# Kernel tuning notes

Hardware: AMD Instinct MI355X
Metric: run time of the kernel (lower is better)

Reference implementation:

```python
import jax, jax.numpy as jnp
import numpy as np

D_MODEL = 1024
N_HEADS = 16
HEAD = D_MODEL // N_HEADS  # 64


def setup_inputs() -> dict:
    key = jax.random.key(0)
    ks = jax.random.split(key, 9)
    s = 1.0 / np.sqrt(D_MODEL)
    x = jax.random.normal(ks[0], (2, 2048, D_MODEL), dtype=jnp.float32)
    Wq = jax.random.uniform(ks[1], (N_HEADS, D_MODEL, HEAD), jnp.float32, -s, s)
    bq = jax.random.uniform(ks[2], (N_HEADS, HEAD), jnp.float32, -s, s)
    Wk = jax.random.uniform(ks[3], (N_HEADS, D_MODEL, HEAD), jnp.float32, -s, s)
    bk = jax.random.uniform(ks[4], (N_HEADS, HEAD), jnp.float32, -s, s)
    Wv = jax.random.uniform(ks[5], (N_HEADS, D_MODEL, HEAD), jnp.float32, -s, s)
    bv = jax.random.uniform(ks[6], (N_HEADS, HEAD), jnp.float32, -s, s)
    Wo = jax.random.uniform(ks[7], (D_MODEL, D_MODEL), jnp.float32, -s, s)
    bo = jax.random.uniform(ks[8], (D_MODEL,), jnp.float32, -s, s)
    return {"x": x, "Wq": Wq, "bq": bq, "Wk": Wk, "bk": bk,
            "Wv": Wv, "bv": bv, "Wo": Wo, "bo": bo}


def reference(x, Wq, bq, Wk, bk, Wv, bv, Wo, bo):
    # Per-head projections, vectorized over heads: [B,S,D] x [H,D,h] -> [B,H,S,h]
    Q = jnp.einsum('bsd,hdk->bhsk', x, Wq) + bq[None, :, None, :]
    K = jnp.einsum('bsd,hdk->bhsk', x, Wk) + bk[None, :, None, :]
    V = jnp.einsum('bsd,hdk->bhsk', x, Wv) + bv[None, :, None, :]
    scores = jnp.einsum('bhqk,bhsk->bhqs', Q, K) / jnp.sqrt(jnp.float32(HEAD))
    attn = jax.nn.softmax(scores, axis=-1)  # dropout is identity in eval mode
    out = jnp.einsum('bhqs,bhsk->bhqk', attn, V)  # [B,H,S,h]
    B, H, S, h = out.shape
    out = out.transpose(0, 2, 1, 3).reshape(B, S, H * h)  # concat heads -> [B,S,D]
    return out @ Wo.T + bo if False else jnp.einsum('bsd,ed->bse', out, Wo.T.T) + bo
```

## Files before the change

### kernel.cpp

```cpp
#include <hip/hip_runtime.h>
#include <hip/hip_bf16.h>

typedef unsigned short u16;
typedef short short8 __attribute__((ext_vector_type(8)));
typedef float floatx4 __attribute__((ext_vector_type(4)));

#define MFMA16(a, b, c) __builtin_amdgcn_mfma_f32_16x16x32_bf16((a), (b), (c), 0, 0, 0)

union U128u { uint4 q; u16 s[8]; };

__device__ __forceinline__ u16 f2bf(float f) {
  union { float f; unsigned u; } v; v.f = f;
  unsigned r = v.u + 0x7fffu + ((v.u >> 16) & 1u);
  return (u16)(r >> 16);
}

__device__ __forceinline__ float bf2f(u16 s) {
  union { unsigned u; float f; } v; v.u = ((unsigned)s) << 16;
  return v.f;
}

__device__ __forceinline__ unsigned pk2(float hi, float lo) {
  union { float f; unsigned u; } a, b;
  a.f = hi; b.f = lo;
  return __builtin_amdgcn_perm(a.u + 0x8000u, b.u + 0x8000u, 0x07060302u);
}

__device__ __forceinline__ float fexp2(float x) {
#if __has_builtin(__builtin_amdgcn_exp2f)
  return __builtin_amdgcn_exp2f(x);
#else
  return exp2f(x);
#endif
}

__device__ __forceinline__ void async16(const u16* g, u16* l) {
  __builtin_amdgcn_global_load_lds(
      (const __attribute__((address_space(1))) unsigned int*)g,
      (__attribute__((address_space(3))) unsigned int*)l, 16, 0, 0);
}


__global__ __launch_bounds__(256) void prep_all(
    const float* __restrict__ x, const float* __restrict__ Wo,
    const float* __restrict__ Wq, const float* __restrict__ bq,
    const float* __restrict__ Wk, const float* __restrict__ bk,
    const float* __restrict__ Wv, const float* __restrict__ bv,
    u16* __restrict__ Xb, u16* __restrict__ Wob,
    u16* __restrict__ Wt, float* __restrict__ ball) {
  int bid = blockIdx.x;
  int tid = threadIdx.x;
  if (bid < 5120) {
    const float* src = bid < 4096 ? x : Wo;
    u16* dst = bid < 4096 ? Xb : Wob;
    int i = (bid < 4096 ? bid : bid - 4096) * 256 + tid;
    float4 v = ((const float4*)src)[i];
    union { unsigned long long ll; u16 s[4]; } o;
    o.s[0] = f2bf(v.x); o.s[1] = f2bf(v.y); o.s[2] = f2bf(v.z); o.s[3] = f2bf(v.w);
    ((unsigned long long*)dst)[i] = o.ll;
    return;
  }
  int id = (bid - 5120) * 256 + tid;
  int kk4 = id & 15;
  int d = (id >> 4) & 1023;
  int h = (id >> 14) & 15;
  int wsel = id >> 18;
  const float* W = wsel == 0 ? Wq : (wsel == 1 ? Wk : Wv);
  float4 v = *(const float4*)(W + ((size_t)(h * 1024 + d)) * 64 + kk4 * 4);
  int nb = wsel * 1024 + h * 64 + kk4 * 4;
  Wt[(size_t)(nb + 0) * 1024 + d] = f2bf(v.x);
  Wt[(size_t)(nb + 1) * 1024 + d] = f2bf(v.y);
  Wt[(size_t)(nb + 2) * 1024 + d] = f2bf(v.z);
  Wt[(size_t)(nb + 3) * 1024 + d] = f2bf(v.w);
  if (id < 3072) {
    int ws2 = id >> 10, hk = id & 1023;
    const float* bsrc = ws2 == 0 ? bq : (ws2 == 1 ? bk : bv);
    ball[id] = bsrc[hk];
  }
}


__device__ __forceinline__ void store_out(u16* p, float v) { *p = f2bf(v); }
__device__ __forceinline__ void store_out(float* p, float v) { *p = v; }

template <int BN, bool SPLITV, bool TRANS, typename OutT>
__global__ __launch_bounds__(256, 4) void gemm_bt(
    const u16* __restrict__ A, const u16* __restrict__ B,
    const float* __restrict__ bias, OutT* __restrict__ C,
    u16* __restrict__ Vtc,
    int M, int N, int K, int scaleNend, float scaleVal) {
  constexpr int TN = BN / 32;
  __shared__ __attribute__((aligned(16))) u16 As[128 * 64];
  __shared__ __attribute__((aligned(16))) u16 Bs[BN * 64];
  const int tid = threadIdx.x;
  const int w = tid >> 6, lane = tid & 63;
  const int l15 = lane & 15, l4 = lane >> 4;
  const int lin = blockIdx.x;
  const int xcd = lin & 7, sblk = lin >> 3;
  const int bm = xcd * 4 + (sblk & 3);
  const int bn = sblk >> 2;
  const int wm = (w & 1) * 64, wn = (w >> 1) * (BN / 2);

  floatx4 acc[4][TN];
#pragma unroll
  for (int i = 0; i < 4; ++i)
#pragma unroll
    for (int j = 0; j < TN; ++j) acc[i][j] = (floatx4){0.f, 0.f, 0.f, 0.f};

  for (int k0 = 0; k0 < K; k0 += 64) {
    __syncthreads();
#pragma unroll
    for (int j = 0; j < 4; ++j) {
      int i = j * 256 + tid;
      int row = i >> 3, c = (i & 7) ^ (row & 7);
      async16(A + (size_t)(bm * 128 + row) * K + k0 + c * 8, As + (j * 256 + w * 64) * 8);
    }
#pragma unroll
    for (int j = 0; j < BN / 32; ++j) {
      int i = j * 256 + tid;
      int row = i >> 3, c = (i & 7) ^ (row & 7);
      async16(B + (size_t)(bn * BN + row) * K + k0 + c * 8, Bs + (j * 256 + w * 64) * 8);
    }
    __syncthreads();
    const int sw = l15 & 7;
#pragma unroll
    for (int ks = 0; ks < 2; ++ks) {
      short8 af[4], bf[TN];
#pragma unroll
      for (int t = 0; t < 4; ++t)
        af[t] = *(const short8*)(As + (wm + t * 16 + l15) * 64 + (((ks * 4 + l4) ^ sw)) * 8);
#pragma unroll
      for (int t = 0; t < TN; ++t)
        bf[t] = *(const short8*)(Bs + (wn + t * 16 + l15) * 64 + (((ks * 4 + l4) ^ sw)) * 8);
#pragma unroll
      for (int tm = 0; tm < 4; ++tm)
#pragma unroll
        for (int tn = 0; tn < TN; ++tn)
          acc[tm][tn] = TRANS ? MFMA16(bf[tn], af[tm], acc[tm][tn])
                              : MFMA16(af[tm], bf[tn], acc[tm][tn]);
    }
  }

  if (TRANS) {
#pragma unroll
    for (int tn = 0; tn < TN; ++tn) {
      int colb = bn * BN + wn + tn * 16 + l4 * 4;
      float4 bv4 = *(const float4*)(bias + colb);
#pragma unroll
      for (int tm = 0; tm < 4; ++tm) {
        int row = bm * 128 + wm + tm * 16 + l15;
        float4 v;
        v.x = acc[tm][tn][0] + bv4.x;
        v.y = acc[tm][tn][1] + bv4.y;
        v.z = acc[tm][tn][2] + bv4.z;
        v.w = acc[tm][tn][3] + bv4.w;
        *(float4*)((float*)C + (size_t)row * N + colb) = v;
      }
    }
    return;
  }

#pragma unroll
  for (int tn = 0; tn < TN; ++tn) {
    int col = bn * BN + wn + tn * 16 + l15;
    float bv = bias[col];
    float sc = (col < scaleNend) ? scaleVal : 1.0f;
    if (!SPLITV || col < 2048) {
#pragma unroll
      for (int tm = 0; tm < 4; ++tm) {
        int row0 = bm * 128 + wm + tm * 16 + l4 * 4;
#pragma unroll
        for (int r = 0; r < 4; ++r) {
          float v = (acc[tm][tn][r] + bv) * sc;
          store_out(C + (size_t)(row0 + r) * N + col, v);
        }
      }
    } else {
      int hv = (col - 2048) >> 6, d = (col - 2048) & 63;
#pragma unroll
      for (int tm = 0; tm < 4; ++tm) {
        int row0 = bm * 128 + wm + tm * 16 + l4 * 4;
        int bb = row0 >> 11, s0 = row0 & 2047;
        union { unsigned long long ll; u16 s[4]; } o;
#pragma unroll
        for (int r = 0; r < 4; ++r) o.s[r] = f2bf(acc[tm][tn][r] + bv);
        size_t idx = ((((size_t)(bb * 16 + hv) * 128 + (s0 >> 4)) * 2 + ((s0 >> 3) & 1)) * 64 + d) * 8 +
                     (s0 & 7);
        *(unsigned long long*)(Vtc + idx) = o.ll;
      }
    }
  }
}

__global__ __launch_bounds__(256, 4) void gemm_out64(
    const u16* __restrict__ A, const u16* __restrict__ B,
    const float* __restrict__ bias, float* __restrict__ C) {
  __shared__ __attribute__((aligned(16))) u16 As[64 * 64];
  __shared__ __attribute__((aligned(16))) u16 Bs[64 * 64];
  const int tid = threadIdx.x;
  const int w = tid >> 6, lane = tid & 63;
  const int l15 = lane & 15, l4 = lane >> 4;
  const int lin = blockIdx.x;
  const int xcd = lin & 7, sblk = lin >> 3;
  const int bm = xcd * 8 + (sblk & 7);
  const int bn = sblk >> 3;
  const int wm = (w & 1) * 32, wn = (w >> 1) * 32;

  floatx4 acc[2][2];
#pragma unroll
  for (int i = 0; i < 2; ++i)
#pragma unroll
    for (int j = 0; j < 2; ++j) acc[i][j] = (floatx4){0.f, 0.f, 0.f, 0.f};

  for (int k0 = 0; k0 < 1024; k0 += 64) {
    __syncthreads();
#pragma unroll
    for (int j = 0; j < 2; ++j) {
      int i = j * 256 + tid;
      int row = i >> 3, c = (i & 7) ^ (row & 7);
      async16(A + (size_t)(bm * 64 + row) * 1024 + k0 + c * 8, As + (j * 256 + w * 64) * 8);
    }
#pragma unroll
    for (int j = 0; j < 2; ++j) {
      int i = j * 256 + tid;
      int row = i >> 3, c = (i & 7) ^ (row & 7);
      async16(B + (size_t)(bn * 64 + row) * 1024 + k0 + c * 8, Bs + (j * 256 + w * 64) * 8);
    }
    __syncthreads();
    const int sw = l15 & 7;
#pragma unroll
    for (int ks = 0; ks < 2; ++ks) {
      short8 af[2], bf[2];
#pragma unroll
      for (int t = 0; t < 2; ++t)
        af[t] = *(const short8*)(As + (wm + t * 16 + l15) * 64 + (((ks * 4 + l4) ^ sw)) * 8);
#pragma unroll
      for (int t = 0; t < 2; ++t)
        bf[t] = *(const short8*)(Bs + (wn + t * 16 + l15) * 64 + (((ks * 4 + l4) ^ sw)) * 8);
#pragma unroll
      for (int tm = 0; tm < 2; ++tm)
#pragma unroll
        for (int tn = 0; tn < 2; ++tn)
          acc[tm][tn] = MFMA16(bf[tn], af[tm], acc[tm][tn]);
    }
  }

#pragma unroll
  for (int tn = 0; tn < 2; ++tn) {
    int colb = bn * 64 + wn + tn * 16 + l4 * 4;
    float4 bv4 = *(const float4*)(bias + colb);
#pragma unroll
    for (int tm = 0; tm < 2; ++tm) {
      int row = bm * 64 + wm + tm * 16 + l15;
      float4 v;
      v.x = acc[tm][tn][0] + bv4.x;
      v.y = acc[tm][tn][1] + bv4.y;
      v.z = acc[tm][tn][2] + bv4.z;
      v.w = acc[tm][tn][3] + bv4.w;
      *(float4*)(C + (size_t)row * 1024 + colb) = v;
    }
  }
}

__global__ __launch_bounds__(256, 3) void attn_kernel(const u16* __restrict__ QKV,
                                                      const u16* __restrict__ Vtc,
                                                      u16* __restrict__ Ob) {
  __shared__ __attribute__((aligned(16))) u16 lds[4 * 5120];
  const int tid = threadIdx.x;
  const int w = tid >> 6, lane = tid & 63;
  const int l15 = lane & 15, l4 = lane >> 4;
  const int lin = blockIdx.x;
  const int xcd = lin & 7, sblk = lin >> 3;
  const int bh = xcd * 4 + (sblk & 3);
  const int q0 = (sblk >> 2) * 64;
  const int b = bh >> 4, h = bh & 15;

  u16* const Pw = lds + w * 5120;

  short8 qf[4][2];
  {
    const u16* Qb = QKV + (size_t)(b * 2048 + q0) * 3072 + h * 64;
#pragma unroll
    for (int tq = 0; tq < 4; ++tq)
#pragma unroll
      for (int s = 0; s < 2; ++s)
        qf[tq][s] = *(const short8*)(Qb + (size_t)(tq * 16 + l15) * 3072 + s * 32 + l4 * 8);
  }

  floatx4 Oacc[4][4];
#pragma unroll
  for (int i = 0; i < 4; ++i)
#pragma unroll
    for (int j = 0; j < 4; ++j) Oacc[i][j] = (floatx4){0.f, 0.f, 0.f, 0.f};
  float lpart[4] = {0.f, 0.f, 0.f, 0.f};

  const u16* const Kb = QKV + (size_t)(b * 2048) * 3072 + 1024 + h * 64;
  const u16* const Vw = Vtc + (size_t)bh * 131072 + (size_t)w * 32768;
  const int kw0 = w * 512;

  auto load_kf = [&](int c, short8 kf[2][2]) {
    const int key0 = kw0 + c * 32;
#pragma unroll
    for (int t = 0; t < 2; ++t)
#pragma unroll
      for (int s = 0; s < 2; ++s)
        kf[t][s] = *(const short8*)(Kb + (size_t)(key0 + t * 16 + l15) * 3072 + s * 32 + l4 * 8);
  };

  auto do_st = [&](const short8 kf[2][2], u16* pb) {
#pragma unroll
    for (int t = 0; t < 2; ++t)
#pragma unroll
      for (int tq = 0; tq < 4; ++tq) {
        floatx4 s = (floatx4){0.f, 0.f, 0.f, 0.f};
        s = MFMA16(kf[t][0], qf[tq][0], s);
        s = MFMA16(kf[t][1], qf[tq][1], s);
        float p0 = fexp2(s[0]), p1 = fexp2(s[1]), p2 = fexp2(s[2]), p3 = fexp2(s[3]);
        lpart[tq] += (p0 + p1) + (p2 + p3);
        unsigned lo = pk2(p1, p0), hi = pk2(p3, p2);
        *(unsigned long long*)(pb + (size_t)(tq * 16 + l15) * 40 + t * 16 + l4 * 4) =
            ((unsigned long long)hi << 32) | lo;
      }
  };

  auto do_pv = [&](int c, const u16* pb) {
    short8 vf[4];
#pragma unroll
    for (int td = 0; td < 4; ++td)
      vf[td] = *(const short8*)(Vw + (size_t)c * 2048 + l4 * 512 + (td * 16 + l15) * 8);
    short8 pf[4];
#pragma unroll
    for (int tq = 0; tq < 4; ++tq)
      pf[tq] = *(const short8*)(pb + (size_t)(tq * 16 + l15) * 40 + l4 * 8);
#pragma unroll
    for (int td = 0; td < 4; ++td)
#pragma unroll
      for (int tq = 0; tq < 4; ++tq) Oacc[tq][td] = MFMA16(pf[tq], vf[td], Oacc[tq][td]);
  };

  short8 kfc[2][2];
  load_kf(0, kfc);
  {
    short8 kfn[2][2];
    load_kf(1, kfn);
    do_st(kfc, Pw);
#pragma unroll
    for (int t = 0; t < 2; ++t)
#pragma unroll
      for (int s = 0; s < 2; ++s) kfc[t][s] = kfn[t][s];
  }
#pragma unroll 1
  for (int c = 1; c < 15; ++c) {
    short8 kfn[2][2];
    load_kf(c + 1, kfn);
    do_st(kfc, Pw + (c & 1) * 2560);
    do_pv(c - 1, Pw + ((c - 1) & 1) * 2560);
#pragma unroll
    for (int t = 0; t < 2; ++t)
#pragma unroll
      for (int s = 0; s < 2; ++s) kfc[t][s] = kfn[t][s];
  }
  do_st(kfc, Pw + 2560);
  do_pv(14, Pw);
  do_pv(15, Pw + 2560);

  float lr[4];
#pragma unroll
  for (int tq = 0; tq < 4; ++tq) {
    float l = lpart[tq];
    l += __shfl_xor(l, 16);
    l += __shfl_xor(l, 32);
    lr[tq] = l;
  }

#pragma unroll
  for (int tq = 0; tq < 4; ++tq)
#pragma unroll
    for (int td = 0; td < 4; ++td)
#pragma unroll
      for (int r = 0; r < 4; ++r)
        Pw[(size_t)(tq * 16 + l4 * 4 + r) * 72 + td * 16 + l15] = f2bf(Oacc[tq][td][r]);
  if (l4 == 0) {
    float* Lw = (float*)(Pw + 4608);
#pragma unroll
    for (int tq = 0; tq < 4; ++tq) Lw[tq * 16 + l15] = lr[tq];
  }
  __syncthreads();

  {
    int row = tid >> 2, c0 = (tid & 3) * 16;
    float acc[16];
#pragma unroll
    for (int j = 0; j < 16; ++j) acc[j] = 0.f;
    float lsum = 0.f;
#pragma unroll
    for (int wv = 0; wv < 4; ++wv) {
      const u16* R = lds + wv * 5120;
      lsum += ((const float*)(R + 4608))[row];
      U128u x1, x2;
      x1.q = *(const uint4*)(R + (size_t)row * 72 + c0);
      x2.q = *(const uint4*)(R + (size_t)row * 72 + c0 + 8);
#pragma unroll
      for (int j = 0; j < 8; ++j) { acc[j] += bf2f(x1.s[j]); acc[8 + j] += bf2f(x2.s[j]); }
    }
    float inv = 1.0f / lsum;
    U128u o1, o2;
#pragma unroll
    for (int j = 0; j < 8; ++j) { o1.s[j] = f2bf(acc[j] * inv); o2.s[j] = f2bf(acc[8 + j] * inv); }
    u16* Op = Ob + (size_t)(b * 2048 + q0 + row) * 1024 + h * 64 + c0;
    *(uint4*)Op = o1.q;
    *(uint4*)(Op + 8) = o2.q;
  }
}


extern "C" void kernel_launch(void* const* d_in, const int* in_sizes, int n_in,
                              void* d_out, int out_size, void* d_ws, size_t ws_size,
                              hipStream_t stream) {
  const float* x  = (const float*)d_in[0];
  const float* Wq = (const float*)d_in[1];
  const float* bq = (const float*)d_in[2];
  const float* Wk = (const float*)d_in[3];
  const float* bk = (const float*)d_in[4];
  const float* Wv = (const float*)d_in[5];
  const float* bv = (const float*)d_in[6];
  const float* Wo = (const float*)d_in[7];
  const float* bo = (const float*)d_in[8];

  char* p = (char*)d_ws;
  u16* Xb   = (u16*)p; p += (size_t)4096 * 1024 * 2;
  u16* Wt   = (u16*)p; p += (size_t)3072 * 1024 * 2;
  u16* QKV  = (u16*)p; p += (size_t)4096 * 3072 * 2;
  u16* Vtc  = (u16*)p; p += (size_t)32 * 128 * 2 * 64 * 8 * 2;
  u16* Ob   = (u16*)p; p += (size_t)4096 * 1024 * 2;
  u16* Wob  = (u16*)p; p += (size_t)1024 * 1024 * 2;
  float* ball = (float*)p; p += 3072 * sizeof(float);

  const float qscale = 0.125f * 1.4426950408889634f;

  prep_all<<<8192, 256, 0, stream>>>(x, Wo, Wq, bq, Wk, bk, Wv, bv, Xb, Wob, Wt, ball);
  gemm_bt<96, true, false, u16><<<1024, 256, 0, stream>>>(Xb, Wt, ball, QKV, Vtc,
                                                          4096, 3072, 1024, 1024, qscale);
  attn_kernel<<<1024, 256, 0, stream>>>(QKV, Vtc, Ob);
  gemm_out64<<<1024, 256, 0, stream>>>(Ob, Wob, bo, (float*)d_out);
}
```

Before: 192.2 us.

## Tile weight transpose through LDS and compute softmax row sums with MFMA

The weight-prep kernel now transposes Wq/Wk/Wv in 128x64 tiles staged in shared memory, so the scattered 2-byte global stores become 16-byte coalesced stores, and the grid shrinks accordingly. In attention, the row sums of the probabilities now come from an extra MFMA against a ones vector instead of scalar adds and cross-lane shuffles. The softmax sum is therefore taken from the bf16-rounded probabilities, which slightly changes numerics. The manual register prefetch of K fragments is also removed and the loads are left to the compiler's scheduling.

Result: no change. 194.8 us (+1.4%).

```diff
diff --git a/kernel.cpp b/kernel.cpp
--- a/kernel.cpp
+++ b/kernel.cpp
@@ -48,6 +48,7 @@
     const float* __restrict__ Wv, const float* __restrict__ bv,
     u16* __restrict__ Xb, u16* __restrict__ Wob,
     u16* __restrict__ Wt, float* __restrict__ ball) {
+  __shared__ __attribute__((aligned(16))) u16 T[128 * 68];
   int bid = blockIdx.x;
   int tid = threadIdx.x;
   if (bid < 5120) {
@@ -60,22 +61,38 @@
     ((unsigned long long*)dst)[i] = o.ll;
     return;
   }
-  int id = (bid - 5120) * 256 + tid;
-  int kk4 = id & 15;
-  int d = (id >> 4) & 1023;
-  int h = (id >> 14) & 15;
-  int wsel = id >> 18;
-  const float* W = wsel == 0 ? Wq : (wsel == 1 ? Wk : Wv);
-  float4 v = *(const float4*)(W + ((size_t)(h * 1024 + d)) * 64 + kk4 * 4);
-  int nb = wsel * 1024 + h * 64 + kk4 * 4;
-  Wt[(size_t)(nb + 0) * 1024 + d] = f2bf(v.x);
-  Wt[(size_t)(nb + 1) * 1024 + d] = f2bf(v.y);
-  Wt[(size_t)(nb + 2) * 1024 + d] = f2bf(v.z);
-  Wt[(size_t)(nb + 3) * 1024 + d] = f2bf(v.w);
-  if (id < 3072) {
+  if (bid < 5132) {
+    int id = (bid - 5120) * 256 + tid;
     int ws2 = id >> 10, hk = id & 1023;
     const float* bsrc = ws2 == 0 ? bq : (ws2 == 1 ? bk : bv);
     ball[id] = bsrc[hk];
+    return;
+  }
+  int tb = bid - 5132;
+  int wsel = tb >> 7;
+  int rem = tb & 127;
+  int h = rem >> 3, dblk = rem & 7;
+  const float* W = wsel == 0 ? Wq : (wsel == 1 ? Wk : Wv);
+  const int d0 = dblk * 128;
+#pragma unroll
+  for (int k = 0; k < 8; ++k) {
+    int slot = k * 256 + tid;
+    int d = slot >> 4, c4 = slot & 15;
+    float4 v = *(const float4*)(W + ((size_t)(h * 1024 + d0 + d)) * 64 + c4 * 4);
+    union { unsigned long long ll; u16 s[4]; } o;
+    o.s[0] = f2bf(v.x); o.s[1] = f2bf(v.y); o.s[2] = f2bf(v.z); o.s[3] = f2bf(v.w);
+    *(unsigned long long*)(T + d * 68 + c4 * 4) = o.ll;
+  }
+  __syncthreads();
+#pragma unroll
+  for (int k = 0; k < 4; ++k) {
+    int slot = k * 256 + tid;
+    int kk = slot >> 4, dc = slot & 15;
+    U128u o;
+#pragma unroll
+    for (int j = 0; j < 8; ++j) o.s[j] = T[(dc * 8 + j) * 68 + kk];
+    int n = wsel * 1024 + h * 64 + kk;
+    *(uint4*)(Wt + (size_t)n * 1024 + d0 + dc * 8) = o.q;
   }
 }
 
@@ -292,22 +309,29 @@
   for (int i = 0; i < 4; ++i)
 #pragma unroll
     for (int j = 0; j < 4; ++j) Oacc[i][j] = (floatx4){0.f, 0.f, 0.f, 0.f};
-  float lpart[4] = {0.f, 0.f, 0.f, 0.f};
+  floatx4 acc_l[4];
+#pragma unroll
+  for (int i = 0; i < 4; ++i) acc_l[i] = (floatx4){0.f, 0.f, 0.f, 0.f};
+
+  short8 vone;
+  {
+    u16 one = (l15 == 0) ? (u16)0x3F80 : (u16)0;
+#pragma unroll
+    for (int j = 0; j < 8; ++j) vone[j] = (short)one;
+  }
 
   const u16* const Kb = QKV + (size_t)(b * 2048) * 3072 + 1024 + h * 64;
   const u16* const Vw = Vtc + (size_t)bh * 131072 + (size_t)w * 32768;
   const int kw0 = w * 512;
 
-  auto load_kf = [&](int c, short8 kf[2][2]) {
+  auto do_st = [&](int c, u16* pb) {
     const int key0 = kw0 + c * 32;
+    short8 kf[2][2];
 #pragma unroll
     for (int t = 0; t < 2; ++t)
 #pragma unroll
       for (int s = 0; s < 2; ++s)
         kf[t][s] = *(const short8*)(Kb + (size_t)(key0 + t * 16 + l15) * 3072 + s * 32 + l4 * 8);
-  };
-
-  auto do_st = [&](const short8 kf[2][2], u16* pb) {
 #pragma unroll
     for (int t = 0; t < 2; ++t)
 #pragma unroll
@@ -316,7 +340,6 @@
         s = MFMA16(kf[t][0], qf[tq][0], s);
         s = MFMA16(kf[t][1], qf[tq][1], s);
         float p0 = fexp2(s[0]), p1 = fexp2(s[1]), p2 = fexp2(s[2]), p3 = fexp2(s[3]);
-        lpart[tq] += (p0 + p1) + (p2 + p3);
         unsigned lo = pk2(p1, p0), hi = pk2(p3, p2);
         *(unsigned long long*)(pb + (size_t)(tq * 16 + l15) * 40 + t * 16 + l4 * 4) =
             ((unsigned long long)hi << 32) | lo;
@@ -336,42 +359,17 @@
     for (int td = 0; td < 4; ++td)
 #pragma unroll
       for (int tq = 0; tq < 4; ++tq) Oacc[tq][td] = MFMA16(pf[tq], vf[td], Oacc[tq][td]);
+#pragma unroll
+    for (int tq = 0; tq < 4; ++tq) acc_l[tq] = MFMA16(pf[tq], vone, acc_l[tq]);
   };
 
-  short8 kfc[2][2];
-  load_kf(0, kfc);
-  {
-    short8 kfn[2][2];
-    load_kf(1, kfn);
-    do_st(kfc, Pw);
-#pragma unroll
-    for (int t = 0; t < 2; ++t)
-#pragma unroll
-      for (int s = 0; s < 2; ++s) kfc[t][s] = kfn[t][s];
-  }
+  do_st(0, Pw);
 #pragma unroll 1
-  for (int c = 1; c < 15; ++c) {
-    short8 kfn[2][2];
-    load_kf(c + 1, kfn);
-    do_st(kfc, Pw + (c & 1) * 2560);
+  for (int c = 1; c < 16; ++c) {
+    do_st(c, Pw + (c & 1) * 2560);
     do_pv(c - 1, Pw + ((c - 1) & 1) * 2560);
-#pragma unroll
-    for (int t = 0; t < 2; ++t)
-#pragma unroll
-      for (int s = 0; s < 2; ++s) kfc[t][s] = kfn[t][s];
-  }
-  do_st(kfc, Pw + 2560);
-  do_pv(14, Pw);
+  }
   do_pv(15, Pw + 2560);
-
-  float lr[4];
-#pragma unroll
-  for (int tq = 0; tq < 4; ++tq) {
-    float l = lpart[tq];
-    l += __shfl_xor(l, 16);
-    l += __shfl_xor(l, 32);
-    lr[tq] = l;
-  }
 
 #pragma unroll
   for (int tq = 0; tq < 4; ++tq)
@@ -380,10 +378,12 @@
 #pragma unroll
       for (int r = 0; r < 4; ++r)
         Pw[(size_t)(tq * 16 + l4 * 4 + r) * 72 + td * 16 + l15] = f2bf(Oacc[tq][td][r]);
-  if (l4 == 0) {
+  if (l15 == 0) {
     float* Lw = (float*)(Pw + 4608);
 #pragma unroll
-    for (int tq = 0; tq < 4; ++tq) Lw[tq * 16 + l15] = lr[tq];
+    for (int tq = 0; tq < 4; ++tq)
+#pragma unroll
+      for (int r = 0; r < 4; ++r) Lw[tq * 16 + l4 * 4 + r] = acc_l[tq][r];
   }
   __syncthreads();
 
@@ -438,7 +438,7 @@
 
   const float qscale = 0.125f * 1.4426950408889634f;
 
-  prep_all<<<8192, 256, 0, stream>>>(x, Wo, Wq, bq, Wk, bk, Wv, bv, Xb, Wob, Wt, ball);
+  prep_all<<<5516, 256, 0, stream>>>(x, Wo, Wq, bq, Wk, bk, Wv, bv, Xb, Wob, Wt, ball);
   gemm_bt<96, true, false, u16><<<1024, 256, 0, stream>>>(Xb, Wt, ball, QKV, Vtc,
                                                           4096, 3072, 1024, 1024, qscale);
   attn_kernel<<<1024, 256, 0, stream>>>(QKV, Vtc, Ob);
```
